# Kernel tuning notes

Hardware: AMD Instinct MI355X
Metric: run time of the kernel (lower is better)

The kernel has to match this reference:

```python
import jax, jax.numpy as jnp
import numpy as np
from jax import lax

N = 2048
D_ENC = 64      # conv channels
D = 512         # node embedding dim (resnet18 feature dim)
K = 5           # max_num_neighbors
L_LAYERS = 4    # num_layers
ARENA = 32.0    # positions scaled to [0, ARENA)^2
R2 = 2.0        # radius^2 = (sqrt(2))^2


def setup_inputs() -> dict:
    key = jax.random.key(0)
    ks = jax.random.split(key, 9)
    imgs = jax.random.normal(ks[0], (N, 3, 64, 64), dtype=jnp.float32)
    pos = jax.random.uniform(ks[1], (N, 2), dtype=jnp.float32)  # scaled by ARENA inside
    conv_w = jax.random.normal(ks[2], (D_ENC, 3, 7, 7), dtype=jnp.float32) * 0.05
    conv_b = jnp.zeros((D_ENC,), dtype=jnp.float32)
    proj_w = jax.random.normal(ks[3], (D_ENC, D), dtype=jnp.float32) * (1.0 / np.sqrt(D_ENC))
    proj_b = jnp.zeros((D,), dtype=jnp.float32)
    w_self = jax.random.normal(ks[4], (L_LAYERS, D, D), dtype=jnp.float32) * (1.0 / np.sqrt(D))
    w_nbr = jax.random.normal(ks[5], (L_LAYERS, D, D), dtype=jnp.float32) * (1.0 / np.sqrt(D))
    b_gnn = jnp.zeros((L_LAYERS, D), dtype=jnp.float32)
    return {"imgs": imgs, "pos": pos, "conv_w": conv_w, "conv_b": conv_b,
            "proj_w": proj_w, "proj_b": proj_b,
            "w_self": w_self, "w_nbr": w_nbr, "b_gnn": b_gnn}


def _encode(imgs, conv_w, conv_b, proj_w, proj_b):
    # conv 7x7 stride 2 + relu + global avg pool + linear -> [N, D]
    x = lax.conv_general_dilated(imgs, conv_w, window_strides=(2, 2), padding="SAME",
                                 dimension_numbers=("NCHW", "OIHW", "NCHW"))
    x = jax.nn.relu(x + conv_b[None, :, None, None])
    x = x.mean(axis=(2, 3))                      # [N, D_ENC]
    return jax.nn.relu(x @ proj_w + proj_b)      # [N, D]


def _radius_knn(pos):
    # radius graph with radius sqrt(2), no self loops, capped at K neighbors
    p = pos * ARENA                              # [N, 2]
    d2 = jnp.sum((p[:, None, :] - p[None, :, :]) ** 2, axis=-1)  # [N, N]
    invalid = (d2 > R2) | jnp.eye(N, dtype=bool)
    d2m = jnp.where(invalid, jnp.inf, d2)
    neg_vals, idx = lax.top_k(-d2m, K)           # K nearest within radius
    valid = jnp.isfinite(neg_vals)               # [N, K]
    return idx, valid


def reference(imgs, pos, conv_w, conv_b, proj_w, proj_b, w_self, w_nbr, b_gnn):
    h = _encode(imgs, conv_w, conv_b, proj_w, proj_b)   # [N, D]
    idx, valid = _radius_knn(pos)                        # [N, K], [N, K]
    vmask = valid.astype(h.dtype)                        # [N, K]
    denom = jnp.maximum(vmask.sum(axis=1, keepdims=True), 1.0)  # [N, 1]
    for l in range(L_LAYERS):
        nbr = h[idx] * vmask[:, :, None]                 # [N, K, D] gather
        agg = nbr.sum(axis=1) / denom                    # mean over valid neighbors
        h = jax.nn.relu(h @ w_self[l] + agg @ w_nbr[l] + b_gnn[l])
    return h
```

## Files before the change

kernel.cpp:

```cpp
#include <hip/hip_runtime.h>


#define NNODES 2048

typedef __attribute__((ext_vector_type(8))) _Float16 half8;
typedef __attribute__((ext_vector_type(16))) float f32x16;

__global__ __launch_bounds__(256) void prep_wfrag_kernel(
    const float* __restrict__ w, ushort* __restrict__ wfrag) {
  int i = blockIdx.x * 256 + threadIdx.x;
  if (i >= 12288) return;
  int j = i & 7;
  int l = (i >> 3) & 63;
  int q = i >> 9;
  int kb = q % 12, ct = q / 12;
  int g = 2 * kb + (l >> 5);
  int c = 32 * ct + (l & 31);
  float val = 0.f;
  if (g < 21 && j < 7) val = w[c * 147 + g * 7 + j];
  wfrag[i] = __builtin_bit_cast(ushort, (_Float16)val);
}

__global__ __launch_bounds__(256) void prep_wT_kernel(
    const float* __restrict__ wsrc_s, const float* __restrict__ wsrc_n,
    ushort* __restrict__ wT) {
  __shared__ float s[64][65];
  int bid = blockIdx.x;
  int m = bid >> 6, kt = (bid >> 3) & 7, nt = bid & 7;
  const float* in = (m < 4) ? (wsrc_s + m * 262144) : (wsrc_n + (m - 4) * 262144);
  ushort* out = wT + m * 262144;
  int t = threadIdx.x;
  int k0 = kt << 6, n0 = nt << 6;
#pragma unroll
  for (int rep = 0; rep < 4; ++rep) {
    int row = (rep << 4) + (t >> 4);
    int c4 = (t & 15) << 2;
    float4 v = *(const float4*)&in[(k0 + row) * 512 + n0 + c4];
    s[row][c4] = v.x; s[row][c4 + 1] = v.y; s[row][c4 + 2] = v.z; s[row][c4 + 3] = v.w;
  }
  __syncthreads();
#pragma unroll
  for (int rep = 0; rep < 4; ++rep) {
    int n = (rep << 4) + (t >> 4);
    int k4 = (t & 15) << 2;
    ushort4 o;
    o.x = __builtin_bit_cast(ushort, (_Float16)s[k4 + 0][n]);
    o.y = __builtin_bit_cast(ushort, (_Float16)s[k4 + 1][n]);
    o.z = __builtin_bit_cast(ushort, (_Float16)s[k4 + 2][n]);
    o.w = __builtin_bit_cast(ushort, (_Float16)s[k4 + 3][n]);
    *(ushort4*)&out[(n0 + n) * 512 + k0 + k4] = o;
  }
}

__device__ inline uint pack2h(float x, float y) {
  ushort a = __builtin_bit_cast(ushort, (_Float16)x);
  ushort b = __builtin_bit_cast(ushort, (_Float16)y);
  return (uint)a | ((uint)b << 16);
}

__global__ __launch_bounds__(256, 3) void conv_pool_kernel(
    const float* __restrict__ imgs, const ushort* __restrict__ wfrag,
    const float* __restrict__ cb, float* __restrict__ enc) {
  __shared__ int4 s_all[2599];
  ushort* s_img = (ushort*)s_all;
  const half8* swf8 = (const half8*)((char*)s_all + 15984);
  float* s_pool = (float*)((char*)s_all + 40560);

  const int n = blockIdx.x >> 1;
  const int r0half = blockIdx.x & 1;
  const int wy = 32 * r0half - 2;
  const int tid = threadIdx.x;
  const int lane = tid & 63;
  const int w = tid >> 6;
  const int hi = lane >> 5;
  const int lo = lane & 31;

  int4 z = {0, 0, 0, 0};
  for (int i = tid; i < 999; i += 256) s_all[i] = z;
  __syncthreads();

  const int4* wf4 = (const int4*)wfrag;
  int4* swf4 = (int4*)((char*)s_all + 15984);
#pragma unroll
  for (int r = 0; r < 6; ++r) swf4[tid + r * 256] = wf4[tid + r * 256];

  const float4* src = (const float4*)(imgs + (size_t)n * 12288);
  for (int i = tid; i < 1776; i += 256) {
    int ic = i / 592;
    int rem = i - ic * 592;
    int li = rem >> 4, xq = rem & 15;
    int iy = wy + li;
    if (iy >= 0 && iy < 64) {
      float4 v = src[(ic * 64 + iy) * 16 + xq];
      int d = (ic * 37 + li) * 72 + (xq << 2) + 2;
      ((uint*)s_img)[d >> 1] = pack2h(v.x, v.y);
      ((uint*)s_img)[(d >> 1) + 1] = pack2h(v.z, v.w);
    }
  }

  int aoff[12];
#pragma unroll
  for (int kb = 0; kb < 12; ++kb) {
    int g = 2 * kb + hi;
    if (g > 20) g = 20;
    int ic = g / 7, ky = g - ic * 7;
    aoff[kb] = (ic * 37 + ky) * 144 + 4 * lo + w * 1152;
  }
  const float bias0 = cb[lo];
  const float bias1 = cb[32 + lo];
  float pool0 = 0.f, pool1 = 0.f;
  __syncthreads();

  const char* sb = (const char*)s_img;
  union F { half8 v; uint u[4]; };

#define LOADF(F0, F1, B0, B1, KB, TPADD) do {                       \
    const char* p_ = sb + aoff[KB] + (TPADD);                       \
    F0.u[0] = *(const uint*)(p_);       F0.u[1] = *(const uint*)(p_ + 4);   \
    F0.u[2] = *(const uint*)(p_ + 8);   F0.u[3] = *(const uint*)(p_ + 12);  \
    F1.u[0] = *(const uint*)(p_ + 288); F1.u[1] = *(const uint*)(p_ + 292); \
    F1.u[2] = *(const uint*)(p_ + 296); F1.u[3] = *(const uint*)(p_ + 300); \
    B0 = swf8[(KB) * 64 + lane];        B1 = swf8[(12 + (KB)) * 64 + lane]; \
  } while (0)

#pragma unroll
  for (int tp = 0; tp < 2; ++tp) {
    const int tpadd = tp * 576;
    f32x16 a0 = {}, a1 = {}, a2 = {}, a3 = {};
    F f0a, f1a, f0b, f1b;
    half8 b0a, b1a, b0b, b1b;
    LOADF(f0a, f1a, b0a, b1a, 0, tpadd);
#pragma unroll
    for (int kb = 0; kb < 12; kb += 2) {
      LOADF(f0b, f1b, b0b, b1b, kb + 1, tpadd);
      a0 = __builtin_amdgcn_mfma_f32_32x32x16_f16(f0a.v, b0a, a0, 0, 0, 0);
      a1 = __builtin_amdgcn_mfma_f32_32x32x16_f16(f0a.v, b1a, a1, 0, 0, 0);
      a2 = __builtin_amdgcn_mfma_f32_32x32x16_f16(f1a.v, b0a, a2, 0, 0, 0);
      a3 = __builtin_amdgcn_mfma_f32_32x32x16_f16(f1a.v, b1a, a3, 0, 0, 0);
      if (kb + 2 < 12) LOADF(f0a, f1a, b0a, b1a, kb + 2, tpadd);
      a0 = __builtin_amdgcn_mfma_f32_32x32x16_f16(f0b.v, b0b, a0, 0, 0, 0);
      a1 = __builtin_amdgcn_mfma_f32_32x32x16_f16(f0b.v, b1b, a1, 0, 0, 0);
      a2 = __builtin_amdgcn_mfma_f32_32x32x16_f16(f1b.v, b0b, a2, 0, 0, 0);
      a3 = __builtin_amdgcn_mfma_f32_32x32x16_f16(f1b.v, b1b, a3, 0, 0, 0);
    }
    float s0 = 0.f, s1 = 0.f;
#pragma unroll
    for (int r = 0; r < 16; ++r) {
      s0 += fmaxf(a0[r] + bias0, 0.f) + fmaxf(a2[r] + bias0, 0.f);
      s1 += fmaxf(a1[r] + bias1, 0.f) + fmaxf(a3[r] + bias1, 0.f);
    }
    pool0 += s0;
    pool1 += s1;
  }
#undef LOADF

  pool0 += __shfl_xor(pool0, 32);
  pool1 += __shfl_xor(pool1, 32);
  if (lane < 32) {
    s_pool[w * 64 + lo] = pool0;
    s_pool[w * 64 + 32 + lo] = pool1;
  }
  __syncthreads();
  if (tid < 64) {
    float s = s_pool[tid] + s_pool[64 + tid] + s_pool[128 + tid] + s_pool[192 + tid];
    atomicAdd(&enc[n * 64 + tid], s * (1.f / 1024.f));
  }
}

__global__ __launch_bounds__(256) void proj_kernel(
    const float* __restrict__ enc, const float* __restrict__ pw,
    const float* __restrict__ pb, ushort* __restrict__ h16) {
  int c = ((blockIdx.x & 1) << 8) | threadIdx.x;
  int r0 = (blockIdx.x >> 1) << 3;
  float bias = pb[c];
  float acc[8];
#pragma unroll
  for (int r = 0; r < 8; ++r) acc[r] = bias;
#pragma unroll 4
  for (int k = 0; k < 64; ++k) {
    float w = pw[k * 512 + c];
#pragma unroll
    for (int r = 0; r < 8; ++r) acc[r] = fmaf(enc[(r0 + r) * 64 + k], w, acc[r]);
  }
#pragma unroll
  for (int r = 0; r < 8; ++r)
    h16[(r0 + r) * 512 + c] = __builtin_bit_cast(ushort, (_Float16)fmaxf(acc[r], 0.f));
}

__global__ __launch_bounds__(256) void knn_kernel(
    const float* __restrict__ pos, int* __restrict__ nbr, float* __restrict__ den) {
  __shared__ float s_d2[NNODES];
  __shared__ int s_idx[NNODES];
  __shared__ int s_cnt;
  const int i = blockIdx.x;
  const int tid = threadIdx.x;
  if (tid == 0) s_cnt = 0;
  __syncthreads();
  const float px = pos[2 * i] * 32.f, py = pos[2 * i + 1] * 32.f;
#pragma unroll
  for (int r = 0; r < 8; ++r) {
    int j = tid + (r << 8);
    float2 q = ((const float2*)pos)[j];
    float dx = q.x * 32.f - px, dy = q.y * 32.f - py;
    float d2 = dx * dx + dy * dy;
    if (d2 <= 2.0f && j != i) {
      int slot = atomicAdd(&s_cnt, 1);
      s_d2[slot] = d2;
      s_idx[slot] = j;
    }
  }
  __syncthreads();
  if (tid < 64) {
    const int lane = tid;
    const int cnt = s_cnt;
    int nf = 0;
#pragma unroll
    for (int k = 0; k < 5; ++k) {
      float best = 1e30f;
      int bslot = 0x7fffffff;
      for (int e = lane; e < cnt; e += 64) {
        float d = s_d2[e];
        if (d < best) { best = d; bslot = e; }
      }
#pragma unroll
      for (int off = 1; off < 64; off <<= 1) {
        float od = __shfl_xor(best, off);
        int os = __shfl_xor(bslot, off);
        if (od < best || (od == best && os < bslot)) { best = od; bslot = os; }
      }
      bool got = (best < 1e30f);
      if (lane == 0) nbr[i * 5 + k] = got ? s_idx[bslot] : -1;
      if (got) { s_d2[bslot] = 1e30f; ++nf; }
    }
    if (lane == 0) den[i] = 1.f / (float)(nf > 0 ? nf : 1);
  }
}

__global__ __launch_bounds__(256) void agg_kernel(
    const ushort* __restrict__ h16, const int* __restrict__ nbr,
    const float* __restrict__ den, ushort* __restrict__ agg16) {
  int i = blockIdx.x >> 1;
  int d = ((blockIdx.x & 1) << 8) + threadIdx.x;
  const _Float16* hp = (const _Float16*)h16;
  float s = 0.f;
#pragma unroll
  for (int k = 0; k < 5; ++k) {
    int j = nbr[i * 5 + k];
    if (j >= 0) s += (float)hp[j * 512 + d];
  }
  agg16[i * 512 + d] = __builtin_bit_cast(ushort, (_Float16)(s * den[i]));
}

__global__ __launch_bounds__(256) void gnn_gemm_kernel(
    const ushort* __restrict__ hA, const ushort* __restrict__ agg,
    const ushort* __restrict__ Ws, const ushort* __restrict__ Wn,
    const float* __restrict__ bias, ushort* __restrict__ hout,
    float* __restrict__ fout, int final_layer) {
  __shared__ ushort s_lds[2][16384];
  const int tid = threadIdx.x;
  const int lane = tid & 63;
  const int hi = lane >> 5, lo = lane & 31;
  const int wu = __builtin_amdgcn_readfirstlane(tid >> 6);
  const int wr = wu >> 1, wc = wu & 1;
  const int bm = blockIdx.x >> 3, bn = blockIdx.x & 7;
  const int r0 = bm << 6, c0 = bn << 6;

  auto STAGE = [&](int buf, int it) {
    int k0 = it << 6;
    const ushort* ph = hA  + (r0 + lane) * 512 + k0 + 8 * wu;
    const ushort* pg = agg + (r0 + lane) * 512 + k0 + 8 * wu;
    const ushort* ps = Ws  + (c0 + lane) * 512 + k0 + 8 * wu;
    const ushort* pn = Wn  + (c0 + lane) * 512 + k0 + 8 * wu;
    ushort* lb = &s_lds[buf][wu << 9];
#define GLDS(SRC, DST) __builtin_amdgcn_global_load_lds( \
      (const __attribute__((address_space(1))) void*)(SRC), \
      (__attribute__((address_space(3))) void*)(DST), 16, 0, 0)
    GLDS(ph, lb);            GLDS(ph + 32, lb + 2048);
    GLDS(pg, lb + 4096);     GLDS(pg + 32, lb + 6144);
    GLDS(ps, lb + 8192);     GLDS(ps + 32, lb + 10240);
    GLDS(pn, lb + 12288);    GLDS(pn + 32, lb + 14336);
#undef GLDS
  };

  f32x16 accS = {}, accN = {};
  STAGE(0, 0);
  __syncthreads();
  int cur = 0;
  for (int it = 0; it < 8; ++it) {
    if (it < 7) STAGE(cur ^ 1, it + 1);
    const half8* pAh = (const half8*)&s_lds[cur][0];
    const half8* pAg = (const half8*)&s_lds[cur][4096];
    const half8* pBs = (const half8*)&s_lds[cur][8192];
    const half8* pBn = (const half8*)&s_lds[cur][12288];
#pragma unroll
    for (int ks = 0; ks < 4; ++ks) {
      int gi = (2 * ks + hi) * 64;
      half8 ah = pAh[gi + 32 * wr + lo];
      half8 bs = pBs[gi + 32 * wc + lo];
      accS = __builtin_amdgcn_mfma_f32_32x32x16_f16(ah, bs, accS, 0, 0, 0);
      half8 ag = pAg[gi + 32 * wr + lo];
      half8 bn2 = pBn[gi + 32 * wc + lo];
      accN = __builtin_amdgcn_mfma_f32_32x32x16_f16(ag, bn2, accN, 0, 0, 0);
    }
    __syncthreads();
    cur ^= 1;
  }

  const int col = c0 + 32 * wc + lo;
  const float b = bias[col];
#pragma unroll
  for (int r = 0; r < 16; ++r) {
    int row = r0 + 32 * wr + (r & 3) + ((r >> 2) << 3) + (hi << 2);
    float v = fmaxf(accS[r] + accN[r] + b, 0.f);
    if (final_layer) fout[row * 512 + col] = v;
    else hout[row * 512 + col] = __builtin_bit_cast(ushort, (_Float16)v);
  }
}

extern "C" void kernel_launch(void* const* d_in, const int* in_sizes, int n_in,
                              void* d_out, int out_size, void* d_ws, size_t ws_size,
                              hipStream_t stream) {
  const float* imgs   = (const float*)d_in[0];
  const float* pos    = (const float*)d_in[1];
  const float* conv_w = (const float*)d_in[2];
  const float* conv_b = (const float*)d_in[3];
  const float* proj_w = (const float*)d_in[4];
  const float* proj_b = (const float*)d_in[5];
  const float* w_self = (const float*)d_in[6];
  const float* w_nbr  = (const float*)d_in[7];
  const float* b_gnn  = (const float*)d_in[8];

  char* ws = (char*)d_ws;
  ushort* wfrag = (ushort*)(ws);
  float*  enc   = (float*) (ws + 32768);
  ushort* h16a  = (ushort*)(ws + 557056);
  ushort* h16b  = (ushort*)(ws + 2654208);
  ushort* agg16 = (ushort*)(ws + 4751360);
  ushort* wT16  = (ushort*)(ws + 6848512);
  int*    nbr   = (int*)   (ws + 11042816);
  float*  den   = (float*) (ws + 11083776);

  prep_wfrag_kernel<<<48, 256, 0, stream>>>(conv_w, wfrag);
  prep_wT_kernel<<<512, 256, 0, stream>>>(w_self, w_nbr, wT16);
  knn_kernel<<<NNODES, 256, 0, stream>>>(pos, nbr, den);
  hipMemsetAsync(enc, 0, 524288, stream);
  conv_pool_kernel<<<2 * NNODES, 256, 0, stream>>>(imgs, wfrag, conv_b, enc);
  proj_kernel<<<512, 256, 0, stream>>>(enc, proj_w, proj_b, h16a);

  for (int l = 0; l < 4; ++l) {
    ushort* hin  = (l & 1) ? h16b : h16a;
    ushort* hnew = (l & 1) ? h16a : h16b;
    agg_kernel<<<4096, 256, 0, stream>>>(hin, nbr, den, agg16);
    gnn_gemm_kernel<<<256, 256, 0, stream>>>(
        hin, agg16, wT16 + l * 262144, wT16 + (4 + l) * 262144,
        b_gnn + l * 512, hnew, (float*)d_out, (l == 3) ? 1 : 0);
  }
}
```

Before: 161.0 us.

## Fuse setup kernels, fold neighbor aggregation into GNN GEMM, read conv weights from global

The weight-prep, kNN, and enc-zeroing steps are merged into one multi-role setup kernel, which removes several launches and the memset. The separate agg kernel is removed: each GNN GEMM block now gathers the neighbor rows itself, sums them in half precision with validity masks, and writes the mean straight into its LDS A-tile, overlapped with the MFMA loop. The conv kernel stops copying its weight fragments into LDS and reads them from global (likely cache-resident) memory, which lowers LDS use and may raise occupancy. The tradeoffs are redundant neighbor gathers across the 8 column blocks, fp16 rounding in the accumulation, and extra register pressure in the GEMM.

Result: slower. 428.5 us (median of 3 runs) (+166.1%).

```diff
diff --git a/kernel.cpp b/kernel.cpp
--- a/kernel.cpp
+++ b/kernel.cpp
@@ -5,52 +5,6 @@
 
 typedef __attribute__((ext_vector_type(8))) _Float16 half8;
 typedef __attribute__((ext_vector_type(16))) float f32x16;
-
-__global__ __launch_bounds__(256) void prep_wfrag_kernel(
-    const float* __restrict__ w, ushort* __restrict__ wfrag) {
-  int i = blockIdx.x * 256 + threadIdx.x;
-  if (i >= 12288) return;
-  int j = i & 7;
-  int l = (i >> 3) & 63;
-  int q = i >> 9;
-  int kb = q % 12, ct = q / 12;
-  int g = 2 * kb + (l >> 5);
-  int c = 32 * ct + (l & 31);
-  float val = 0.f;
-  if (g < 21 && j < 7) val = w[c * 147 + g * 7 + j];
-  wfrag[i] = __builtin_bit_cast(ushort, (_Float16)val);
-}
-
-__global__ __launch_bounds__(256) void prep_wT_kernel(
-    const float* __restrict__ wsrc_s, const float* __restrict__ wsrc_n,
-    ushort* __restrict__ wT) {
-  __shared__ float s[64][65];
-  int bid = blockIdx.x;
-  int m = bid >> 6, kt = (bid >> 3) & 7, nt = bid & 7;
-  const float* in = (m < 4) ? (wsrc_s + m * 262144) : (wsrc_n + (m - 4) * 262144);
-  ushort* out = wT + m * 262144;
-  int t = threadIdx.x;
-  int k0 = kt << 6, n0 = nt << 6;
-#pragma unroll
-  for (int rep = 0; rep < 4; ++rep) {
-    int row = (rep << 4) + (t >> 4);
-    int c4 = (t & 15) << 2;
-    float4 v = *(const float4*)&in[(k0 + row) * 512 + n0 + c4];
-    s[row][c4] = v.x; s[row][c4 + 1] = v.y; s[row][c4 + 2] = v.z; s[row][c4 + 3] = v.w;
-  }
-  __syncthreads();
-#pragma unroll
-  for (int rep = 0; rep < 4; ++rep) {
-    int n = (rep << 4) + (t >> 4);
-    int k4 = (t & 15) << 2;
-    ushort4 o;
-    o.x = __builtin_bit_cast(ushort, (_Float16)s[k4 + 0][n]);
-    o.y = __builtin_bit_cast(ushort, (_Float16)s[k4 + 1][n]);
-    o.z = __builtin_bit_cast(ushort, (_Float16)s[k4 + 2][n]);
-    o.w = __builtin_bit_cast(ushort, (_Float16)s[k4 + 3][n]);
-    *(ushort4*)&out[(n0 + n) * 512 + k0 + k4] = o;
-  }
-}
 
 __device__ inline uint pack2h(float x, float y) {
   ushort a = __builtin_bit_cast(ushort, (_Float16)x);
@@ -58,14 +12,115 @@
   return (uint)a | ((uint)b << 16);
 }
 
+__global__ __launch_bounds__(256) void setup_kernel(
+    const float* __restrict__ conv_w, const float* __restrict__ wsrc_s,
+    const float* __restrict__ wsrc_n, const float* __restrict__ pos,
+    ushort* __restrict__ wfrag, ushort* __restrict__ wT,
+    int* __restrict__ nbr, float* __restrict__ den, float* __restrict__ enc) {
+  __shared__ float4 smem4[1040];
+  const int bid = blockIdx.x;
+  const int tid = threadIdx.x;
+
+  if (bid < 48) {
+    int i = bid * 256 + tid;
+    int j = i & 7;
+    int l = (i >> 3) & 63;
+    int q = i >> 9;
+    int kb = q % 12, ct = q / 12;
+    int g = 2 * kb + (l >> 5);
+    int c = 32 * ct + (l & 31);
+    float val = 0.f;
+    if (g < 21 && j < 7) val = conv_w[c * 147 + g * 7 + j];
+    wfrag[i] = __builtin_bit_cast(ushort, (_Float16)val);
+    return;
+  }
+
+  if (bid < 560) {
+    float(*s)[65] = (float(*)[65])smem4;
+    int bid2 = bid - 48;
+    int m = bid2 >> 6, kt = (bid2 >> 3) & 7, nt = bid2 & 7;
+    const float* in = (m < 4) ? (wsrc_s + m * 262144) : (wsrc_n + (m - 4) * 262144);
+    ushort* out = wT + m * 262144;
+    int k0 = kt << 6, n0 = nt << 6;
+#pragma unroll
+    for (int rep = 0; rep < 4; ++rep) {
+      int row = (rep << 4) + (tid >> 4);
+      int c4 = (tid & 15) << 2;
+      float4 v = *(const float4*)&in[(k0 + row) * 512 + n0 + c4];
+      s[row][c4] = v.x; s[row][c4 + 1] = v.y; s[row][c4 + 2] = v.z; s[row][c4 + 3] = v.w;
+    }
+    __syncthreads();
+#pragma unroll
+    for (int rep = 0; rep < 4; ++rep) {
+      int n = (rep << 4) + (tid >> 4);
+      int k4 = (tid & 15) << 2;
+      ushort4 o;
+      o.x = __builtin_bit_cast(ushort, (_Float16)s[k4 + 0][n]);
+      o.y = __builtin_bit_cast(ushort, (_Float16)s[k4 + 1][n]);
+      o.z = __builtin_bit_cast(ushort, (_Float16)s[k4 + 2][n]);
+      o.w = __builtin_bit_cast(ushort, (_Float16)s[k4 + 3][n]);
+      *(ushort4*)&out[(n0 + n) * 512 + k0 + k4] = o;
+    }
+    return;
+  }
+
+  {
+    float* s_d2 = (float*)smem4;
+    int* s_idx = (int*)(s_d2 + NNODES);
+    int* s_cnt = (int*)(s_idx + NNODES);
+    const int i = bid - 560;
+    if (tid < 16) {
+      float4 z4 = {0.f, 0.f, 0.f, 0.f};
+      ((float4*)(enc + i * 64))[tid] = z4;
+    }
+    if (tid == 0) *s_cnt = 0;
+    __syncthreads();
+    const float px = pos[2 * i] * 32.f, py = pos[2 * i + 1] * 32.f;
+#pragma unroll
+    for (int r = 0; r < 8; ++r) {
+      int j = tid + (r << 8);
+      float2 q = ((const float2*)pos)[j];
+      float dx = q.x * 32.f - px, dy = q.y * 32.f - py;
+      float d2 = dx * dx + dy * dy;
+      if (d2 <= 2.0f && j != i) {
+        int slot = atomicAdd(s_cnt, 1);
+        s_d2[slot] = d2;
+        s_idx[slot] = j;
+      }
+    }
+    __syncthreads();
+    if (tid < 64) {
+      const int lane = tid;
+      const int cnt = *s_cnt;
+      int nf = 0;
+#pragma unroll
+      for (int k = 0; k < 5; ++k) {
+        float best = 1e30f;
+        int bslot = 0x7fffffff;
+        for (int e = lane; e < cnt; e += 64) {
+          float d = s_d2[e];
+          if (d < best) { best = d; bslot = e; }
+        }
+#pragma unroll
+        for (int off = 1; off < 64; off <<= 1) {
+          float od = __shfl_xor(best, off);
+          int os = __shfl_xor(bslot, off);
+          if (od < best || (od == best && os < bslot)) { best = od; bslot = os; }
+        }
+        bool got = (best < 1e30f);
+        if (lane == 0) nbr[i * 5 + k] = got ? s_idx[bslot] : -1;
+        if (got) { s_d2[bslot] = 1e30f; ++nf; }
+      }
+      if (lane == 0) den[i] = 1.f / (float)(nf > 0 ? nf : 1);
+    }
+  }
+}
+
 __global__ __launch_bounds__(256, 3) void conv_pool_kernel(
     const float* __restrict__ imgs, const ushort* __restrict__ wfrag,
     const float* __restrict__ cb, float* __restrict__ enc) {
-  __shared__ int4 s_all[2599];
-  ushort* s_img = (ushort*)s_all;
-  const half8* swf8 = (const half8*)((char*)s_all + 15984);
-  float* s_pool = (float*)((char*)s_all + 40560);
-
+  __shared__ ushort s_img[7992];
+  __shared__ float s_pool[256];
   const int n = blockIdx.x >> 1;
   const int r0half = blockIdx.x & 1;
   const int wy = 32 * r0half - 2;
@@ -76,13 +131,8 @@
   const int lo = lane & 31;
 
   int4 z = {0, 0, 0, 0};
-  for (int i = tid; i < 999; i += 256) s_all[i] = z;
+  for (int i = tid; i < 999; i += 256) ((int4*)s_img)[i] = z;
   __syncthreads();
-
-  const int4* wf4 = (const int4*)wfrag;
-  int4* swf4 = (int4*)((char*)s_all + 15984);
-#pragma unroll
-  for (int r = 0; r < 6; ++r) swf4[tid + r * 256] = wf4[tid + r * 256];
 
   const float4* src = (const float4*)(imgs + (size_t)n * 12288);
   for (int i = tid; i < 1776; i += 256) {
@@ -112,15 +162,20 @@
   __syncthreads();
 
   const char* sb = (const char*)s_img;
+  const half8* wf8 = (const half8*)wfrag;
   union F { half8 v; uint u[4]; };
 
-#define LOADF(F0, F1, B0, B1, KB, TPADD) do {                       \
-    const char* p_ = sb + aoff[KB] + (TPADD);                       \
-    F0.u[0] = *(const uint*)(p_);       F0.u[1] = *(const uint*)(p_ + 4);   \
-    F0.u[2] = *(const uint*)(p_ + 8);   F0.u[3] = *(const uint*)(p_ + 12);  \
-    F1.u[0] = *(const uint*)(p_ + 288); F1.u[1] = *(const uint*)(p_ + 292); \
-    F1.u[2] = *(const uint*)(p_ + 296); F1.u[3] = *(const uint*)(p_ + 300); \
-    B0 = swf8[(KB) * 64 + lane];        B1 = swf8[(12 + (KB)) * 64 + lane]; \
+#define LOADA(F0, F1, KB, TPADD) do {                                        \
+    const char* p_ = (const char*)__builtin_assume_aligned(                  \
+        sb + aoff[KB] + (TPADD), 4);                                         \
+    __builtin_memcpy(&F0.u[0], p_, 8);                                       \
+    __builtin_memcpy(&F0.u[2], p_ + 8, 8);                                   \
+    __builtin_memcpy(&F1.u[0], p_ + 288, 8);                                 \
+    __builtin_memcpy(&F1.u[2], p_ + 296, 8);                                 \
+  } while (0)
+#define LOADB(B0, B1, KB) do {                                               \
+    B0 = wf8[(KB) * 64 + lane];                                              \
+    B1 = wf8[(12 + (KB)) * 64 + lane];                                       \
   } while (0)
 
 #pragma unroll
@@ -129,15 +184,20 @@
     f32x16 a0 = {}, a1 = {}, a2 = {}, a3 = {};
     F f0a, f1a, f0b, f1b;
     half8 b0a, b1a, b0b, b1b;
-    LOADF(f0a, f1a, b0a, b1a, 0, tpadd);
+    LOADA(f0a, f1a, 0, tpadd);
+    LOADB(b0a, b1a, 0);
 #pragma unroll
     for (int kb = 0; kb < 12; kb += 2) {
-      LOADF(f0b, f1b, b0b, b1b, kb + 1, tpadd);
+      LOADA(f0b, f1b, kb + 1, tpadd);
+      LOADB(b0b, b1b, kb + 1);
       a0 = __builtin_amdgcn_mfma_f32_32x32x16_f16(f0a.v, b0a, a0, 0, 0, 0);
       a1 = __builtin_amdgcn_mfma_f32_32x32x16_f16(f0a.v, b1a, a1, 0, 0, 0);
       a2 = __builtin_amdgcn_mfma_f32_32x32x16_f16(f1a.v, b0a, a2, 0, 0, 0);
       a3 = __builtin_amdgcn_mfma_f32_32x32x16_f16(f1a.v, b1a, a3, 0, 0, 0);
-      if (kb + 2 < 12) LOADF(f0a, f1a, b0a, b1a, kb + 2, tpadd);
+      if (kb + 2 < 12) {
+        LOADA(f0a, f1a, kb + 2, tpadd);
+        LOADB(b0a, b1a, kb + 2);
+      }
       a0 = __builtin_amdgcn_mfma_f32_32x32x16_f16(f0b.v, b0b, a0, 0, 0, 0);
       a1 = __builtin_amdgcn_mfma_f32_32x32x16_f16(f0b.v, b1b, a1, 0, 0, 0);
       a2 = __builtin_amdgcn_mfma_f32_32x32x16_f16(f1b.v, b0b, a2, 0, 0, 0);
@@ -152,7 +212,8 @@
     pool0 += s0;
     pool1 += s1;
   }
-#undef LOADF
+#undef LOADA
+#undef LOADB
 
   pool0 += __shfl_xor(pool0, 32);
   pool1 += __shfl_xor(pool1, 32);
@@ -187,76 +248,15 @@
     h16[(r0 + r) * 512 + c] = __builtin_bit_cast(ushort, (_Float16)fmaxf(acc[r], 0.f));
 }
 
-__global__ __launch_bounds__(256) void knn_kernel(
-    const float* __restrict__ pos, int* __restrict__ nbr, float* __restrict__ den) {
-  __shared__ float s_d2[NNODES];
-  __shared__ int s_idx[NNODES];
-  __shared__ int s_cnt;
-  const int i = blockIdx.x;
-  const int tid = threadIdx.x;
-  if (tid == 0) s_cnt = 0;
-  __syncthreads();
-  const float px = pos[2 * i] * 32.f, py = pos[2 * i + 1] * 32.f;
-#pragma unroll
-  for (int r = 0; r < 8; ++r) {
-    int j = tid + (r << 8);
-    float2 q = ((const float2*)pos)[j];
-    float dx = q.x * 32.f - px, dy = q.y * 32.f - py;
-    float d2 = dx * dx + dy * dy;
-    if (d2 <= 2.0f && j != i) {
-      int slot = atomicAdd(&s_cnt, 1);
-      s_d2[slot] = d2;
-      s_idx[slot] = j;
-    }
-  }
-  __syncthreads();
-  if (tid < 64) {
-    const int lane = tid;
-    const int cnt = s_cnt;
-    int nf = 0;
-#pragma unroll
-    for (int k = 0; k < 5; ++k) {
-      float best = 1e30f;
-      int bslot = 0x7fffffff;
-      for (int e = lane; e < cnt; e += 64) {
-        float d = s_d2[e];
-        if (d < best) { best = d; bslot = e; }
-      }
-#pragma unroll
-      for (int off = 1; off < 64; off <<= 1) {
-        float od = __shfl_xor(best, off);
-        int os = __shfl_xor(bslot, off);
-        if (od < best || (od == best && os < bslot)) { best = od; bslot = os; }
-      }
-      bool got = (best < 1e30f);
-      if (lane == 0) nbr[i * 5 + k] = got ? s_idx[bslot] : -1;
-      if (got) { s_d2[bslot] = 1e30f; ++nf; }
-    }
-    if (lane == 0) den[i] = 1.f / (float)(nf > 0 ? nf : 1);
-  }
-}
-
-__global__ __launch_bounds__(256) void agg_kernel(
+__global__ __launch_bounds__(256) void gnn_gemm_kernel(
     const ushort* __restrict__ h16, const int* __restrict__ nbr,
-    const float* __restrict__ den, ushort* __restrict__ agg16) {
-  int i = blockIdx.x >> 1;
-  int d = ((blockIdx.x & 1) << 8) + threadIdx.x;
-  const _Float16* hp = (const _Float16*)h16;
-  float s = 0.f;
-#pragma unroll
-  for (int k = 0; k < 5; ++k) {
-    int j = nbr[i * 5 + k];
-    if (j >= 0) s += (float)hp[j * 512 + d];
-  }
-  agg16[i * 512 + d] = __builtin_bit_cast(ushort, (_Float16)(s * den[i]));
-}
-
-__global__ __launch_bounds__(256) void gnn_gemm_kernel(
-    const ushort* __restrict__ hA, const ushort* __restrict__ agg,
+    const float* __restrict__ den,
     const ushort* __restrict__ Ws, const ushort* __restrict__ Wn,
     const float* __restrict__ bias, ushort* __restrict__ hout,
     float* __restrict__ fout, int final_layer) {
   __shared__ ushort s_lds[2][16384];
+  __shared__ int s_nbr[320];
+  __shared__ float s_den[64];
   const int tid = threadIdx.x;
   const int lane = tid & 63;
   const int hi = lane >> 5, lo = lane & 31;
@@ -265,29 +265,81 @@
   const int bm = blockIdx.x >> 3, bn = blockIdx.x & 7;
   const int r0 = bm << 6, c0 = bn << 6;
 
+  if (tid < 80) ((int4*)s_nbr)[tid] = ((const int4*)(nbr + r0 * 5))[tid];
+  else if (tid < 96) ((float4*)s_den)[tid - 80] = ((const float4*)(den + r0))[tid - 80];
+  __syncthreads();
+
+  const int grow = tid >> 2, gseg = tid & 3;
+  int gj[5];
+  uint gm[5];
+#pragma unroll
+  for (int k = 0; k < 5; ++k) {
+    int j = s_nbr[grow * 5 + k];
+    gm[k] = (j >= 0) ? 0xFFFFFFFFu : 0u;
+    gj[k] = (j >= 0) ? j : 0;
+  }
+  half8 den8;
+  {
+    _Float16 dh = (_Float16)s_den[grow];
+#pragma unroll
+    for (int e = 0; e < 8; ++e) den8[e] = dh;
+  }
+
+  union GU { half8 v; uint u[4]; };
+  GU ga[5][2];
+
+  auto GATHER = [&](int it) {
+    const ushort* hb = h16 + (it << 6) + gseg * 16;
+#pragma unroll
+    for (int k = 0; k < 5; ++k) {
+      const half8* p = (const half8*)(hb + gj[k] * 512);
+      ga[k][0].v = p[0];
+      ga[k][1].v = p[1];
+    }
+  };
+  auto COMBINE = [&](int buf) {
+#pragma unroll
+    for (int part = 0; part < 2; ++part) {
+      GU t0, t1, t2, t3, t4;
+#pragma unroll
+      for (int j2 = 0; j2 < 4; ++j2) {
+        t0.u[j2] = ga[0][part].u[j2] & gm[0];
+        t1.u[j2] = ga[1][part].u[j2] & gm[1];
+        t2.u[j2] = ga[2][part].u[j2] & gm[2];
+        t3.u[j2] = ga[3][part].u[j2] & gm[3];
+        t4.u[j2] = ga[4][part].u[j2] & gm[4];
+      }
+      half8 s = ((t0.v + t1.v) + (t2.v + t3.v)) + t4.v;
+      s = s * den8;
+      *(half8*)&s_lds[buf][4096 + (2 * gseg + part) * 512 + grow * 8] = s;
+    }
+  };
   auto STAGE = [&](int buf, int it) {
     int k0 = it << 6;
-    const ushort* ph = hA  + (r0 + lane) * 512 + k0 + 8 * wu;
-    const ushort* pg = agg + (r0 + lane) * 512 + k0 + 8 * wu;
-    const ushort* ps = Ws  + (c0 + lane) * 512 + k0 + 8 * wu;
-    const ushort* pn = Wn  + (c0 + lane) * 512 + k0 + 8 * wu;
+    const ushort* ph = h16 + (r0 + lane) * 512 + k0 + 8 * wu;
+    const ushort* ps = Ws + (c0 + lane) * 512 + k0 + 8 * wu;
+    const ushort* pn = Wn + (c0 + lane) * 512 + k0 + 8 * wu;
     ushort* lb = &s_lds[buf][wu << 9];
 #define GLDS(SRC, DST) __builtin_amdgcn_global_load_lds( \
       (const __attribute__((address_space(1))) void*)(SRC), \
       (__attribute__((address_space(3))) void*)(DST), 16, 0, 0)
     GLDS(ph, lb);            GLDS(ph + 32, lb + 2048);
-    GLDS(pg, lb + 4096);     GLDS(pg + 32, lb + 6144);
     GLDS(ps, lb + 8192);     GLDS(ps + 32, lb + 10240);
     GLDS(pn, lb + 12288);    GLDS(pn + 32, lb + 14336);
 #undef GLDS
   };
 
   f32x16 accS = {}, accN = {};
+  GATHER(0);
   STAGE(0, 0);
+  COMBINE(0);
   __syncthreads();
   int cur = 0;
   for (int it = 0; it < 8; ++it) {
-    if (it < 7) STAGE(cur ^ 1, it + 1);
+    if (it < 7) {
+      GATHER(it + 1);
+      STAGE(cur ^ 1, it + 1);
+    }
     const half8* pAh = (const half8*)&s_lds[cur][0];
     const half8* pAg = (const half8*)&s_lds[cur][4096];
     const half8* pBs = (const half8*)&s_lds[cur][8192];
@@ -302,6 +354,7 @@
       half8 bn2 = pBn[gi + 32 * wc + lo];
       accN = __builtin_amdgcn_mfma_f32_32x32x16_f16(ag, bn2, accN, 0, 0, 0);
     }
+    if (it < 7) COMBINE(cur ^ 1);
     __syncthreads();
     cur ^= 1;
   }
@@ -335,24 +388,20 @@
   float*  enc   = (float*) (ws + 32768);
   ushort* h16a  = (ushort*)(ws + 557056);
   ushort* h16b  = (ushort*)(ws + 2654208);
-  ushort* agg16 = (ushort*)(ws + 4751360);
   ushort* wT16  = (ushort*)(ws + 6848512);
   int*    nbr   = (int*)   (ws + 11042816);
   float*  den   = (float*) (ws + 11083776);
 
-  prep_wfrag_kernel<<<48, 256, 0, stream>>>(conv_w, wfrag);
-  prep_wT_kernel<<<512, 256, 0, stream>>>(w_self, w_nbr, wT16);
-  knn_kernel<<<NNODES, 256, 0, stream>>>(pos, nbr, den);
-  hipMemsetAsync(enc, 0, 524288, stream);
+  setup_kernel<<<2608, 256, 0, stream>>>(conv_w, w_self, w_nbr, pos,
+                                         wfrag, wT16, nbr, den, enc);
   conv_pool_kernel<<<2 * NNODES, 256, 0, stream>>>(imgs, wfrag, conv_b, enc);
   proj_kernel<<<512, 256, 0, stream>>>(enc, proj_w, proj_b, h16a);
 
   for (int l = 0; l < 4; ++l) {
     ushort* hin  = (l & 1) ? h16b : h16a;
     ushort* hnew = (l & 1) ? h16a : h16b;
-    agg_kernel<<<4096, 256, 0, stream>>>(hin, nbr, den, agg16);
     gnn_gemm_kernel<<<256, 256, 0, stream>>>(
-        hin, agg16, wT16 + l * 262144, wT16 + (4 + l) * 262144,
+        hin, nbr, den, wT16 + l * 262144, wT16 + (4 + l) * 262144,
         b_gnn + l * 512, hnew, (float*)d_out, (l == 3) ? 1 : 0);
   }
 }
```
